# Optimization experiments

Hardware: AMD Instinct MI355X
Metric: run time of the kernel (lower is better)

Reference implementation:

```python
import jax, jax.numpy as jnp
import numpy as np

N = 50000   # nodes
E = 800000  # edges (avg degree 16)
IN, H, OUT = 128, 256, 40


def setup_inputs() -> dict:
    key = jax.random.key(0)
    ks = jax.random.split(key, 7)
    x = jax.random.normal(ks[0], (N, IN), dtype=jnp.float32)
    edge_index = jax.random.randint(ks[1], (2, E), 0, N, dtype=jnp.int32)
    def w(k, fi, fo):
        return jax.random.normal(k, (fi, fo), dtype=jnp.float32) / np.sqrt(fi).astype(np.float32)
    return {
        "x": x,
        "edge_index": edge_index,
        "W0": w(ks[2], IN, H), "b0": jnp.zeros((H,), jnp.float32),
        "W1": w(ks[3], H, H),  "b1": jnp.zeros((H,), jnp.float32),
        "W2": w(ks[4], H, H),  "b2": jnp.zeros((H,), jnp.float32),
        "Wh": w(ks[5], H, OUT), "bh": jnp.zeros((OUT,), jnp.float32),
    }


def gcn_conv(x, src, dst, W, b, n):
    """PyG GCNConv: self-loops + symmetric D^-1/2 (A+I) D^-1/2 normalization."""
    h = x @ W  # [N, Fout]
    # degree with self-loop (edge weights are all 1)
    deg = jnp.ones((n,), h.dtype).at[dst].add(1.0)
    inv = jax.lax.rsqrt(deg)  # deg^{-1/2}
    coef = inv[src] * inv[dst]  # [E]
    agg = jax.ops.segment_sum(h[src] * coef[:, None], dst, num_segments=n)
    agg = agg + h * (inv * inv)[:, None]  # self-loop contribution
    return agg + b


def reference(x, edge_index, W0, b0, W1, b1, W2, b2, Wh, bh):
    src, dst = edge_index[0], edge_index[1]
    h = jax.nn.relu(gcn_conv(x, src, dst, W0, b0, N))   # conv0 + relu (dropout p=0)
    h = jax.nn.relu(gcn_conv(h, src, dst, W1, b1, N))   # conv1 + relu
    h = gcn_conv(h, src, dst, W2, b2, N)                # final conv (no relu)
    g = jnp.mean(h, axis=0, keepdims=True)              # batch=None -> global mean, [1, H]
    return g @ Wh + bh                                  # prediction head, [1, OUT]
```

## Files before the change

kernel.cpp:

```cpp
#include <hip/hip_runtime.h>

#define NN 50000
#define NE 800000
#define FIN 128
#define FH 256
#define FOUT 40
#define NPAD 50432
#define NN2 50048
#define NB 256
#define BSPAN 196
#define EBLK 4096
#define NBLK_A 196
#define NBLK_S 196

typedef float f32x4 __attribute__((ext_vector_type(4)));
typedef short bf16x8 __attribute__((ext_vector_type(8)));

__device__ __forceinline__ ushort f2bf(float f) {
    unsigned u = __float_as_uint(f);
    unsigned r = (u + 0x7FFFu + ((u >> 16) & 1u)) >> 16;
    return (ushort)r;
}
__device__ __forceinline__ float bf2f(ushort b) {
    return __uint_as_float(((unsigned)b) << 16);
}


__global__ __launch_bounds__(256) void bucket_cnt_kernel(const int* __restrict__ dst,
                                                         int* __restrict__ bcnt) {
    __shared__ int h[NB];
    const int t = threadIdx.x;
    h[t] = 0;
    __syncthreads();
    const int e0 = blockIdx.x * EBLK;
    const int n  = min(EBLK, NE - e0);
    for (int i = t; i < n; i += 256)
        atomicAdd(&h[dst[e0 + i] / BSPAN], 1);
    __syncthreads();
    if (h[t] > 0) atomicAdd(&bcnt[t], h[t]);
}

__global__ __launch_bounds__(256) void bucket_scan_kernel(const int* __restrict__ bcnt,
                                                          int* __restrict__ bbase,
                                                          int* __restrict__ bcur,
                                                          float* __restrict__ vbuf) {
    __shared__ int sh[256];
    int t = threadIdx.x;
    int v = bcnt[t];
    sh[t] = v;
    __syncthreads();
    #pragma unroll
    for (int off = 1; off < 256; off <<= 1) {
        int u = (t >= off) ? sh[t - off] : 0;
        __syncthreads();
        sh[t] += u;
        __syncthreads();
    }
    int excl = sh[t] - v;
    bbase[t] = excl;
    bcur[t]  = excl;
    if (t == 255) bbase[256] = sh[255];
    vbuf[t] = 0.0f;
}

__global__ __launch_bounds__(256) void binA_kernel(const int* __restrict__ src,
                                                   const int* __restrict__ dst,
                                                   int* __restrict__ bcur,
                                                   unsigned* __restrict__ inter) {
    __shared__ int hcnt[NB];
    __shared__ int hoff[NB];
    __shared__ int lcur[NB];
    __shared__ int gbase[NB];
    __shared__ unsigned stage[EBLK];

    const int t  = threadIdx.x;
    const int e0 = blockIdx.x * EBLK;
    const int n  = min(EBLK, NE - e0);

    hcnt[t] = 0;
    __syncthreads();
    for (int i = t; i < n; i += 256)
        atomicAdd(&hcnt[dst[e0 + i] / BSPAN], 1);
    __syncthreads();
    int v = hcnt[t];
    hoff[t] = v;
    __syncthreads();
    #pragma unroll
    for (int off = 1; off < NB; off <<= 1) {
        int u = (t >= off) ? hoff[t - off] : 0;
        __syncthreads();
        hoff[t] += u;
        __syncthreads();
    }
    int excl = hoff[t] - v;
    __syncthreads();
    hoff[t] = excl;
    lcur[t] = excl;
    if (v > 0) gbase[t] = atomicAdd(&bcur[t], v);
    __syncthreads();
    for (int i = t; i < n; i += 256) {
        int d = dst[e0 + i];
        int s = src[e0 + i];
        int b = d / BSPAN;
        int idx = atomicAdd(&lcur[b], 1);
        stage[idx] = ((unsigned)d << 16) | (unsigned)s;
    }
    __syncthreads();
    for (int i = t; i < n; i += 256) {
        unsigned rec = stage[i];
        int b = (int)(rec >> 16) / BSPAN;
        inter[gbase[b] + (i - hoff[b])] = rec;
    }
}

__global__ __launch_bounds__(256) void binB1_kernel(const unsigned* __restrict__ inter,
                                                    const int* __restrict__ bbase,
                                                    int* __restrict__ row_start,
                                                    float* __restrict__ inv,
                                                    float* __restrict__ wsum) {
    __shared__ int lcnt[BSPAN];
    __shared__ int sh[256];
    const int b   = blockIdx.x;
    const int nlo = b * BSPAN;
    const int nhi = min(nlo + BSPAN, NN);
    const int nn  = nhi - nlo;
    const int base = bbase[b];
    const int cnt  = bbase[b + 1] - base;
    const int t = threadIdx.x;

    for (int i = t; i < nn; i += 256) lcnt[i] = 0;
    __syncthreads();
    for (int i = t; i < cnt; i += 256)
        atomicAdd(&lcnt[(int)(inter[base + i] >> 16) - nlo], 1);
    __syncthreads();
    int c = (t < nn) ? lcnt[t] : 0;
    sh[t] = c;
    __syncthreads();
    #pragma unroll
    for (int off = 1; off < 256; off <<= 1) {
        int u = (t >= off) ? sh[t - off] : 0;
        __syncthreads();
        sh[t] += u;
        __syncthreads();
    }
    if (t < nn) {
        row_start[nlo + t] = base + sh[t] - c;
        inv[nlo + t]  = rsqrtf((float)(c + 1));
        wsum[nlo + t] = 0.0f;
    }
    if (b == NB - 1 && t == 0) row_start[NN] = NE;
}

__global__ __launch_bounds__(256) void binB2_kernel(const unsigned* __restrict__ inter,
                                                    const int* __restrict__ bbase,
                                                    const int* __restrict__ row_start,
                                                    const float* __restrict__ inv,
                                                    float2* __restrict__ edata,
                                                    float* __restrict__ wsum) {
    __shared__ int lcur[BSPAN];
    const int b   = blockIdx.x;
    const int nlo = b * BSPAN;
    const int nhi = min(nlo + BSPAN, NN);
    const int nn  = nhi - nlo;
    const int base = bbase[b];
    const int cnt  = bbase[b + 1] - base;
    const int t = threadIdx.x;

    for (int i = t; i < nn; i += 256) lcur[i] = row_start[nlo + i];
    __syncthreads();
    for (int i = t; i < cnt; i += 256) {
        unsigned rec = inter[base + i];
        int d = (int)(rec >> 16);
        int s = (int)(rec & 0xFFFFu);
        float coef = inv[s] * inv[d];
        int pos = atomicAdd(&lcur[d - nlo], 1);
        edata[pos] = make_float2(__int_as_float(s), coef);
        unsafeAtomicAdd(&wsum[s], coef);
    }
}


__global__ void wsplit_kernel(const float* __restrict__ W, int K, int N,
                              ushort* __restrict__ WtH, ushort* __restrict__ WtL) {
    int idx = blockIdx.x * 256 + threadIdx.x;
    if (idx >= K * N) return;
    int n = idx % N;
    int k = idx / N;
    float f = W[idx];
    ushort h = f2bf(f);
    WtH[(size_t)n * K + k] = h;
    if (WtL) WtL[(size_t)n * K + k] = f2bf(f - bf2f(h));
}


template<int TERMS, bool BIAS_RELU>
__global__ __launch_bounds__(256) void gemm_mfma_kernel(
    const ushort* __restrict__ AH, const ushort* __restrict__ AL,
    const ushort* __restrict__ BH, const ushort* __restrict__ BL,
    const float* __restrict__ bias,
    ushort* __restrict__ outB,
    int M, int K) {
    constexpr int NARR = (TERMS == 3) ? 4 : 2;
    __shared__ ushort smem[NARR * 128 * 40];
    ushort* Ah = smem;
    ushort* Bh = smem + 128 * 40;
    ushort* Al = (TERMS == 3) ? smem + 2 * 128 * 40 : nullptr;
    ushort* Bl = (TERMS == 3) ? smem + 3 * 128 * 40 : nullptr;

    const int tid  = threadIdx.x;
    const int lane = tid & 63;
    const int w    = tid >> 6;
    const int wr   = w >> 1;
    const int wc   = w & 1;
    const int row0 = blockIdx.x * 128;
    const int col0 = blockIdx.y * 128;

    f32x4 acc[4][4] = {};

    for (int k0 = 0; k0 < K; k0 += 32) {
        #pragma unroll
        for (int i = 0; i < 2; ++i) {
            int c  = i * 256 + tid;
            int r  = c >> 2;
            int cb = c & 3;
            int gr = row0 + r;
            uint4 vh = make_uint4(0u, 0u, 0u, 0u);
            if (gr < M)
                vh = *reinterpret_cast<const uint4*>(AH + (size_t)gr * K + k0 + cb * 8);
            *reinterpret_cast<uint4*>(&Ah[r * 40 + cb * 8]) = vh;
            *reinterpret_cast<uint4*>(&Bh[r * 40 + cb * 8]) =
                *reinterpret_cast<const uint4*>(BH + (size_t)(col0 + r) * K + k0 + cb * 8);
            if (TERMS == 3) {
                uint4 vl = make_uint4(0u, 0u, 0u, 0u);
                if (gr < M)
                    vl = *reinterpret_cast<const uint4*>(AL + (size_t)gr * K + k0 + cb * 8);
                *reinterpret_cast<uint4*>(&Al[r * 40 + cb * 8]) = vl;
                *reinterpret_cast<uint4*>(&Bl[r * 40 + cb * 8]) =
                    *reinterpret_cast<const uint4*>(BL + (size_t)(col0 + r) * K + k0 + cb * 8);
            }
        }
        __syncthreads();

        const int rsel = lane & 15;
        const int ksel = (lane >> 4) * 8;
        bf16x8 ah[4], bh[4];
        #pragma unroll
        for (int m = 0; m < 4; ++m)
            ah[m] = *reinterpret_cast<const bf16x8*>(&Ah[(wr * 64 + m * 16 + rsel) * 40 + ksel]);
        #pragma unroll
        for (int n = 0; n < 4; ++n)
            bh[n] = *reinterpret_cast<const bf16x8*>(&Bh[(wc * 64 + n * 16 + rsel) * 40 + ksel]);

        if (TERMS == 3) {
            bf16x8 al[4], bl[4];
            #pragma unroll
            for (int m = 0; m < 4; ++m)
                al[m] = *reinterpret_cast<const bf16x8*>(&Al[(wr * 64 + m * 16 + rsel) * 40 + ksel]);
            #pragma unroll
            for (int n = 0; n < 4; ++n)
                bl[n] = *reinterpret_cast<const bf16x8*>(&Bl[(wc * 64 + n * 16 + rsel) * 40 + ksel]);
            #pragma unroll
            for (int m = 0; m < 4; ++m)
                #pragma unroll
                for (int n = 0; n < 4; ++n) {
                    acc[m][n] = __builtin_amdgcn_mfma_f32_16x16x32_bf16(ah[m], bh[n], acc[m][n], 0, 0, 0);
                    acc[m][n] = __builtin_amdgcn_mfma_f32_16x16x32_bf16(ah[m], bl[n], acc[m][n], 0, 0, 0);
                    acc[m][n] = __builtin_amdgcn_mfma_f32_16x16x32_bf16(al[m], bh[n], acc[m][n], 0, 0, 0);
                }
        } else {
            #pragma unroll
            for (int m = 0; m < 4; ++m)
                #pragma unroll
                for (int n = 0; n < 4; ++n)
                    acc[m][n] = __builtin_amdgcn_mfma_f32_16x16x32_bf16(ah[m], bh[n], acc[m][n], 0, 0, 0);
        }
        __syncthreads();
    }

    const int cl = lane & 15;
    const int rg = lane >> 4;
    #pragma unroll
    for (int m = 0; m < 4; ++m) {
        #pragma unroll
        for (int i = 0; i < 4; ++i) {
            int gr = row0 + wr * 64 + m * 16 + rg * 4 + i;
            if (gr < M) {
                #pragma unroll
                for (int n = 0; n < 4; ++n) {
                    int gc = col0 + wc * 64 + n * 16 + cl;
                    float o = acc[m][n][i];
                    if (BIAS_RELU) o = fmaxf(o + bias[gc], 0.0f);
                    outB[(size_t)gr * FH + gc] = f2bf(o);
                }
            }
        }
    }
}


__global__ __launch_bounds__(256) void gather_x_kernel(const float* __restrict__ x,
                                                       const float2* __restrict__ edata,
                                                       const int* __restrict__ row_start,
                                                       const float* __restrict__ inv,
                                                       ushort* __restrict__ outH,
                                                       ushort* __restrict__ outL) {
    int node = blockIdx.x * 4 + (threadIdx.x >> 6);
    int lane = threadIdx.x & 63;
    if (node >= NN) return;

    int beg = row_start[node];
    int end = row_start[node + 1];

    float iv = inv[node];
    float c  = iv * iv;
    float2 v = *reinterpret_cast<const float2*>(x + (size_t)node * FIN + lane * 2);
    float2 a0 = make_float2(v.x * c, v.y * c);
    float2 a1 = make_float2(0.f, 0.f);
    float2 a2 = make_float2(0.f, 0.f);
    float2 a3 = make_float2(0.f, 0.f);

    int i = beg;
    if ((i & 1) && i < end) {
        float2 ed = edata[i];
        float2 w = *reinterpret_cast<const float2*>(x + (size_t)__float_as_int(ed.x) * FIN + lane * 2);
        a0.x += w.x * ed.y; a0.y += w.y * ed.y;
        ++i;
    }
    for (; i + 8 <= end; i += 8) {
        float4 e01 = *reinterpret_cast<const float4*>(&edata[i]);
        float4 e23 = *reinterpret_cast<const float4*>(&edata[i + 2]);
        float4 e45 = *reinterpret_cast<const float4*>(&edata[i + 4]);
        float4 e67 = *reinterpret_cast<const float4*>(&edata[i + 6]);
        float2 w0 = *reinterpret_cast<const float2*>(x + (size_t)__float_as_int(e01.x) * FIN + lane * 2);
        float2 w1 = *reinterpret_cast<const float2*>(x + (size_t)__float_as_int(e01.z) * FIN + lane * 2);
        float2 w2 = *reinterpret_cast<const float2*>(x + (size_t)__float_as_int(e23.x) * FIN + lane * 2);
        float2 w3 = *reinterpret_cast<const float2*>(x + (size_t)__float_as_int(e23.z) * FIN + lane * 2);
        float2 w4 = *reinterpret_cast<const float2*>(x + (size_t)__float_as_int(e45.x) * FIN + lane * 2);
        float2 w5 = *reinterpret_cast<const float2*>(x + (size_t)__float_as_int(e45.z) * FIN + lane * 2);
        float2 w6 = *reinterpret_cast<const float2*>(x + (size_t)__float_as_int(e67.x) * FIN + lane * 2);
        float2 w7 = *reinterpret_cast<const float2*>(x + (size_t)__float_as_int(e67.z) * FIN + lane * 2);
        a0.x += w0.x * e01.y; a0.y += w0.y * e01.y;
        a1.x += w1.x * e01.w; a1.y += w1.y * e01.w;
        a2.x += w2.x * e23.y; a2.y += w2.y * e23.y;
        a3.x += w3.x * e23.w; a3.y += w3.y * e23.w;
        a0.x += w4.x * e45.y; a0.y += w4.y * e45.y;
        a1.x += w5.x * e45.w; a1.y += w5.y * e45.w;
        a2.x += w6.x * e67.y; a2.y += w6.y * e67.y;
        a3.x += w7.x * e67.w; a3.y += w7.y * e67.w;
    }
    for (; i + 2 <= end; i += 2) {
        float4 e01 = *reinterpret_cast<const float4*>(&edata[i]);
        float2 w0 = *reinterpret_cast<const float2*>(x + (size_t)__float_as_int(e01.x) * FIN + lane * 2);
        float2 w1 = *reinterpret_cast<const float2*>(x + (size_t)__float_as_int(e01.z) * FIN + lane * 2);
        a0.x += w0.x * e01.y; a0.y += w0.y * e01.y;
        a1.x += w1.x * e01.w; a1.y += w1.y * e01.w;
    }
    if (i < end) {
        float2 ed = edata[i];
        float2 w = *reinterpret_cast<const float2*>(x + (size_t)__float_as_int(ed.x) * FIN + lane * 2);
        a0.x += w.x * ed.y; a0.y += w.y * ed.y;
    }

    float ax = a0.x + a1.x + a2.x + a3.x;
    float ay = a0.y + a1.y + a2.y + a3.y;
    ushort h0 = f2bf(ax), h1 = f2bf(ay);
    ushort l0 = f2bf(ax - bf2f(h0)), l1 = f2bf(ay - bf2f(h1));
    size_t o = (size_t)node * FIN + lane * 2;
    *reinterpret_cast<ushort2*>(outH + o) = make_ushort2(h0, h1);
    *reinterpret_cast<ushort2*>(outL + o) = make_ushort2(l0, l1);
}


__global__ __launch_bounds__(256) void gather_bf_kernel(const ushort* __restrict__ lin,
                                                        const float2* __restrict__ edata,
                                                        const int* __restrict__ row_start,
                                                        const float* __restrict__ inv,
                                                        const float* __restrict__ bias,
                                                        ushort* __restrict__ outB) {
    int node = blockIdx.x * 4 + (threadIdx.x >> 6);
    int lane = threadIdx.x & 63;
    if (node >= NN) return;

    int beg = row_start[node];
    int end = row_start[node + 1];

    float iv = inv[node];
    float c  = iv * iv;
    ushort4 sv = *reinterpret_cast<const ushort4*>(lin + (size_t)node * FH + lane * 4);
    float4 b = *reinterpret_cast<const float4*>(bias + lane * 4);
    float4 a0 = make_float4(bf2f(sv.x) * c + b.x, bf2f(sv.y) * c + b.y,
                            bf2f(sv.z) * c + b.z, bf2f(sv.w) * c + b.w);
    float4 a1 = make_float4(0.f, 0.f, 0.f, 0.f);
    float4 a2 = make_float4(0.f, 0.f, 0.f, 0.f);
    float4 a3 = make_float4(0.f, 0.f, 0.f, 0.f);

    int i = beg;
    if ((i & 1) && i < end) {
        float2 ed = edata[i];
        float cf = ed.y;
        ushort4 wv = *reinterpret_cast<const ushort4*>(lin + (size_t)__float_as_int(ed.x) * FH + lane * 4);
        a0.x += bf2f(wv.x) * cf; a0.y += bf2f(wv.y) * cf;
        a0.z += bf2f(wv.z) * cf; a0.w += bf2f(wv.w) * cf;
        ++i;
    }
    for (; i + 8 <= end; i += 8) {
        float4 e01 = *reinterpret_cast<const float4*>(&edata[i]);
        float4 e23 = *reinterpret_cast<const float4*>(&edata[i + 2]);
        float4 e45 = *reinterpret_cast<const float4*>(&edata[i + 4]);
        float4 e67 = *reinterpret_cast<const float4*>(&edata[i + 6]);
        ushort4 w0 = *reinterpret_cast<const ushort4*>(lin + (size_t)__float_as_int(e01.x) * FH + lane * 4);
        ushort4 w1 = *reinterpret_cast<const ushort4*>(lin + (size_t)__float_as_int(e01.z) * FH + lane * 4);
        ushort4 w2 = *reinterpret_cast<const ushort4*>(lin + (size_t)__float_as_int(e23.x) * FH + lane * 4);
        ushort4 w3 = *reinterpret_cast<const ushort4*>(lin + (size_t)__float_as_int(e23.z) * FH + lane * 4);
        ushort4 w4 = *reinterpret_cast<const ushort4*>(lin + (size_t)__float_as_int(e45.x) * FH + lane * 4);
        ushort4 w5 = *reinterpret_cast<const ushort4*>(lin + (size_t)__float_as_int(e45.z) * FH + lane * 4);
        ushort4 w6 = *reinterpret_cast<const ushort4*>(lin + (size_t)__float_as_int(e67.x) * FH + lane * 4);
        ushort4 w7 = *reinterpret_cast<const ushort4*>(lin + (size_t)__float_as_int(e67.z) * FH + lane * 4);
        a0.x += bf2f(w0.x) * e01.y; a0.y += bf2f(w0.y) * e01.y;
        a0.z += bf2f(w0.z) * e01.y; a0.w += bf2f(w0.w) * e01.y;
        a1.x += bf2f(w1.x) * e01.w; a1.y += bf2f(w1.y) * e01.w;
        a1.z += bf2f(w1.z) * e01.w; a1.w += bf2f(w1.w) * e01.w;
        a2.x += bf2f(w2.x) * e23.y; a2.y += bf2f(w2.y) * e23.y;
        a2.z += bf2f(w2.z) * e23.y; a2.w += bf2f(w2.w) * e23.y;
        a3.x += bf2f(w3.x) * e23.w; a3.y += bf2f(w3.y) * e23.w;
        a3.z += bf2f(w3.z) * e23.w; a3.w += bf2f(w3.w) * e23.w;
        a0.x += bf2f(w4.x) * e45.y; a0.y += bf2f(w4.y) * e45.y;
        a0.z += bf2f(w4.z) * e45.y; a0.w += bf2f(w4.w) * e45.y;
        a1.x += bf2f(w5.x) * e45.w; a1.y += bf2f(w5.y) * e45.w;
        a1.z += bf2f(w5.z) * e45.w; a1.w += bf2f(w5.w) * e45.w;
        a2.x += bf2f(w6.x) * e67.y; a2.y += bf2f(w6.y) * e67.y;
        a2.z += bf2f(w6.z) * e67.y; a2.w += bf2f(w6.w) * e67.y;
        a3.x += bf2f(w7.x) * e67.w; a3.y += bf2f(w7.y) * e67.w;
        a3.z += bf2f(w7.z) * e67.w; a3.w += bf2f(w7.w) * e67.w;
    }
    for (; i + 2 <= end; i += 2) {
        float4 e01 = *reinterpret_cast<const float4*>(&edata[i]);
        ushort4 w0 = *reinterpret_cast<const ushort4*>(lin + (size_t)__float_as_int(e01.x) * FH + lane * 4);
        ushort4 w1 = *reinterpret_cast<const ushort4*>(lin + (size_t)__float_as_int(e01.z) * FH + lane * 4);
        a0.x += bf2f(w0.x) * e01.y; a0.y += bf2f(w0.y) * e01.y;
        a0.z += bf2f(w0.z) * e01.y; a0.w += bf2f(w0.w) * e01.y;
        a1.x += bf2f(w1.x) * e01.w; a1.y += bf2f(w1.y) * e01.w;
        a1.z += bf2f(w1.z) * e01.w; a1.w += bf2f(w1.w) * e01.w;
    }
    if (i < end) {
        float2 ed = edata[i];
        float cf = ed.y;
        ushort4 wv = *reinterpret_cast<const ushort4*>(lin + (size_t)__float_as_int(ed.x) * FH + lane * 4);
        a0.x += bf2f(wv.x) * cf; a0.y += bf2f(wv.y) * cf;
        a0.z += bf2f(wv.z) * cf; a0.w += bf2f(wv.w) * cf;
    }

    float4 acc = make_float4(a0.x + a1.x + a2.x + a3.x,
                             a0.y + a1.y + a2.y + a3.y,
                             a0.z + a1.z + a2.z + a3.z,
                             a0.w + a1.w + a2.w + a3.w);

    float r0 = fmaxf(acc.x, 0.f), r1 = fmaxf(acc.y, 0.f);
    float r2 = fmaxf(acc.z, 0.f), r3 = fmaxf(acc.w, 0.f);
    *reinterpret_cast<ushort4*>(outB + (size_t)node * FH + lane * 4) =
        make_ushort4(f2bf(r0), f2bf(r1), f2bf(r2), f2bf(r3));
}


__global__ __launch_bounds__(256) void colsumw_kernel(const ushort* __restrict__ a1,
                                                      const float* __restrict__ wsum,
                                                      const float* __restrict__ inv,
                                                      float* __restrict__ v) {
    __shared__ float sh[4][256];
    int wid  = threadIdx.x >> 6;
    int lane = threadIdx.x & 63;
    int r0 = blockIdx.x * 256;
    int r1 = r0 + 256; if (r1 > NN) r1 = NN;

    float4 acc = make_float4(0.f, 0.f, 0.f, 0.f);
    for (int r = r0 + wid; r < r1; r += 4) {
        float iv = inv[r];
        float wr = wsum[r] + iv * iv;
        ushort4 u = *reinterpret_cast<const ushort4*>(a1 + (size_t)r * FH + lane * 4);
        acc.x += bf2f(u.x) * wr;
        acc.y += bf2f(u.y) * wr;
        acc.z += bf2f(u.z) * wr;
        acc.w += bf2f(u.w) * wr;
    }
    *reinterpret_cast<float4*>(&sh[wid][lane * 4]) = acc;
    __syncthreads();
    if (wid == 0) {
        float4 s1 = *reinterpret_cast<const float4*>(&sh[1][lane * 4]);
        float4 s2 = *reinterpret_cast<const float4*>(&sh[2][lane * 4]);
        float4 s3 = *reinterpret_cast<const float4*>(&sh[3][lane * 4]);
        unsafeAtomicAdd(&v[lane * 4 + 0], acc.x + s1.x + s2.x + s3.x);
        unsafeAtomicAdd(&v[lane * 4 + 1], acc.y + s1.y + s2.y + s3.y);
        unsafeAtomicAdd(&v[lane * 4 + 2], acc.z + s1.z + s2.z + s3.z);
        unsafeAtomicAdd(&v[lane * 4 + 3], acc.w + s1.w + s2.w + s3.w);
    }
}

__global__ __launch_bounds__(256) void head2_kernel(const float* __restrict__ v,
                                                    const float* __restrict__ W2,
                                                    const float* __restrict__ b2,
                                                    const float* __restrict__ Wh,
                                                    const float* __restrict__ bh,
                                                    float* __restrict__ out) {
    __shared__ float m[FH];
    int t = threadIdx.x;
    const float scale = 1.0f / (float)NN;
    float s = 0.0f;
    for (int f = 0; f < FH; ++f)
        s += v[f] * W2[f * FH + t];
    m[t] = s * scale + b2[t];
    __syncthreads();
    if (t < FOUT) {
        float o = 0.0f;
        for (int f = 0; f < FH; ++f)
            o += m[f] * Wh[f * FOUT + t];
        out[t] = o + bh[t];
    }
}


extern "C" void kernel_launch(void* const* d_in, const int* in_sizes, int n_in,
                              void* d_out, int out_size, void* d_ws, size_t ws_size,
                              hipStream_t stream) {
    const float* x   = (const float*)d_in[0];
    const int*   ei  = (const int*)d_in[1];
    const float* W0  = (const float*)d_in[2];
    const float* b0  = (const float*)d_in[3];
    const float* W1  = (const float*)d_in[4];
    const float* b1  = (const float*)d_in[5];
    const float* W2  = (const float*)d_in[6];
    const float* b2  = (const float*)d_in[7];
    const float* Wh  = (const float*)d_in[8];
    const float* bh  = (const float*)d_in[9];
    float* out = (float*)d_out;

    const int* src = ei;
    const int* dst = ei + NE;

    float*    inv       = (float*)d_ws;
    int*      row_start = (int*)(inv + NPAD);
    float*    wsum      = (float*)(row_start + NPAD);
    int*      bcnt      = (int*)(wsum + NPAD);
    int*      bbase     = bcnt + 256;
    int*      bcur      = bbase + 320;
    float*    vbuf      = (float*)(bcur + 256);
    unsigned* inter     = (unsigned*)(vbuf + 256);
    float2*   edata     = (float2*)(inter + NE);
    ushort*   W0tH      = (ushort*)(edata + NE);
    ushort*   W0tL      = W0tH + 256 * 128;
    ushort*   W1tH      = W0tL + 256 * 128;
    ushort*   aggxH     = W1tH + 256 * 256;
    ushort*   aggxL     = aggxH + (size_t)NN2 * 128;
    ushort*   linb      = aggxH;
    ushort*   h0H       = aggxL + (size_t)NN2 * 128;
    ushort*   a1H       = h0H;

    const dim3 gemm_grid((NN + 127) / 128, 2);
    const int nblk_g = (NN + 3) / 4;

    hipMemsetAsync(bcnt, 0, NB * sizeof(int), stream);
    bucket_cnt_kernel<<<NBLK_A, 256, 0, stream>>>(dst, bcnt);
    bucket_scan_kernel<<<1, 256, 0, stream>>>(bcnt, bbase, bcur, vbuf);
    binA_kernel<<<NBLK_A, 256, 0, stream>>>(src, dst, bcur, inter);
    binB1_kernel<<<NB, 256, 0, stream>>>(inter, bbase, row_start, inv, wsum);
    binB2_kernel<<<NB, 256, 0, stream>>>(inter, bbase, row_start, inv, edata, wsum);
    wsplit_kernel<<<(FIN * FH + 255) / 256, 256, 0, stream>>>(W0, FIN, FH, W0tH, W0tL);
    wsplit_kernel<<<(FH * FH + 255) / 256, 256, 0, stream>>>(W1, FH, FH, W1tH, nullptr);

    gather_x_kernel<<<nblk_g, 256, 0, stream>>>(x, edata, row_start, inv, aggxH, aggxL);
    gemm_mfma_kernel<3, true><<<gemm_grid, 256, 0, stream>>>(aggxH, aggxL, W0tH, W0tL, b0,
                                                             h0H, NN, FIN);

    gemm_mfma_kernel<1, false><<<gemm_grid, 256, 0, stream>>>(h0H, nullptr, W1tH, nullptr, nullptr,
                                                              linb, NN, FH);
    gather_bf_kernel<<<nblk_g, 256, 0, stream>>>(linb, edata, row_start, inv, b1, a1H);

    colsumw_kernel<<<NBLK_S, 256, 0, stream>>>(a1H, wsum, inv, vbuf);
    head2_kernel<<<1, 256, 0, stream>>>(vbuf, W2, b2, Wh, bh, out);
}
```

Measured before the change: 314.9 us.

## Gather x in bf16, widen GEMM tile to full 256 columns, merge weight splits

Adds a pass that converts x to bf16 (padded to NN2 rows), so the first-layer neighbor gather reads half the bytes per edge. The GEMM now computes all 256 output columns per block (128x256 tile, 4x8 accumulators) over a padded row range, dropping the row bounds checks and the duplicate A-tile loads across column blocks. The two weight-split kernels are merged into one launch. This adds an extra full pass over x and more registers and LDS per GEMM block, and rounding x to bf16 before aggregation adds precision error.

```diff
diff --git a/kernel.cpp b/kernel.cpp
--- a/kernel.cpp
+++ b/kernel.cpp
@@ -180,16 +180,38 @@
 }
 
 
-__global__ void wsplit_kernel(const float* __restrict__ W, int K, int N,
-                              ushort* __restrict__ WtH, ushort* __restrict__ WtL) {
+__global__ void wsplit_all_kernel(const float* __restrict__ W0, const float* __restrict__ W1,
+                                  ushort* __restrict__ W0tH, ushort* __restrict__ W0tL,
+                                  ushort* __restrict__ W1tH) {
     int idx = blockIdx.x * 256 + threadIdx.x;
-    if (idx >= K * N) return;
-    int n = idx % N;
-    int k = idx / N;
-    float f = W[idx];
-    ushort h = f2bf(f);
-    WtH[(size_t)n * K + k] = h;
-    if (WtL) WtL[(size_t)n * K + k] = f2bf(f - bf2f(h));
+    if (idx < FIN * FH) {
+        int n = idx % FH;
+        int k = idx / FH;
+        float f = W0[idx];
+        ushort h = f2bf(f);
+        W0tH[n * FIN + k] = h;
+        W0tL[n * FIN + k] = f2bf(f - bf2f(h));
+    }
+    int j = idx - FIN * FH;
+    if (j >= 0 && j < FH * FH) {
+        int n = j % FH;
+        int k = j / FH;
+        W1tH[n * FH + k] = f2bf(W1[j]);
+    }
+}
+
+
+__global__ void xcvt_kernel(const float* __restrict__ x, ushort* __restrict__ xb) {
+    int t = blockIdx.x * 256 + threadIdx.x;
+    if (t >= NN2 * 32) return;
+    int row = t >> 5;
+    int c4  = t & 31;
+    ushort4 o = make_ushort4(0, 0, 0, 0);
+    if (row < NN) {
+        float4 v = *reinterpret_cast<const float4*>(x + (size_t)row * FIN + c4 * 4);
+        o = make_ushort4(f2bf(v.x), f2bf(v.y), f2bf(v.z), f2bf(v.w));
+    }
+    *reinterpret_cast<ushort4*>(xb + (size_t)row * FIN + c4 * 4) = o;
 }
 
 
@@ -199,13 +221,13 @@
     const ushort* __restrict__ BH, const ushort* __restrict__ BL,
     const float* __restrict__ bias,
     ushort* __restrict__ outB,
-    int M, int K) {
-    constexpr int NARR = (TERMS == 3) ? 4 : 2;
-    __shared__ ushort smem[NARR * 128 * 40];
+    int K) {
+    constexpr int NARR = (TERMS == 3) ? 2 : 1;
+    __shared__ ushort smem[(128 + 256) * 40 * NARR];
     ushort* Ah = smem;
     ushort* Bh = smem + 128 * 40;
-    ushort* Al = (TERMS == 3) ? smem + 2 * 128 * 40 : nullptr;
-    ushort* Bl = (TERMS == 3) ? smem + 3 * 128 * 40 : nullptr;
+    ushort* Al = (TERMS == 3) ? smem + 384 * 40 : nullptr;
+    ushort* Bl = (TERMS == 3) ? smem + 384 * 40 + 128 * 40 : nullptr;
 
     const int tid  = threadIdx.x;
     const int lane = tid & 63;
@@ -213,9 +235,8 @@
     const int wr   = w >> 1;
     const int wc   = w & 1;
     const int row0 = blockIdx.x * 128;
-    const int col0 = blockIdx.y * 128;
-
-    f32x4 acc[4][4] = {};
+
+    f32x4 acc[4][8] = {};
 
     for (int k0 = 0; k0 < K; k0 += 32) {
         #pragma unroll
@@ -223,46 +244,47 @@
             int c  = i * 256 + tid;
             int r  = c >> 2;
             int cb = c & 3;
-            int gr = row0 + r;
-            uint4 vh = make_uint4(0u, 0u, 0u, 0u);
-            if (gr < M)
-                vh = *reinterpret_cast<const uint4*>(AH + (size_t)gr * K + k0 + cb * 8);
-            *reinterpret_cast<uint4*>(&Ah[r * 40 + cb * 8]) = vh;
+            *reinterpret_cast<uint4*>(&Ah[r * 40 + cb * 8]) =
+                *reinterpret_cast<const uint4*>(AH + (size_t)(row0 + r) * K + k0 + cb * 8);
+            if (TERMS == 3)
+                *reinterpret_cast<uint4*>(&Al[r * 40 + cb * 8]) =
+                    *reinterpret_cast<const uint4*>(AL + (size_t)(row0 + r) * K + k0 + cb * 8);
+        }
+        #pragma unroll
+        for (int i = 0; i < 4; ++i) {
+            int c  = i * 256 + tid;
+            int r  = c >> 2;
+            int cb = c & 3;
             *reinterpret_cast<uint4*>(&Bh[r * 40 + cb * 8]) =
-                *reinterpret_cast<const uint4*>(BH + (size_t)(col0 + r) * K + k0 + cb * 8);
-            if (TERMS == 3) {
-                uint4 vl = make_uint4(0u, 0u, 0u, 0u);
-                if (gr < M)
-                    vl = *reinterpret_cast<const uint4*>(AL + (size_t)gr * K + k0 + cb * 8);
-                *reinterpret_cast<uint4*>(&Al[r * 40 + cb * 8]) = vl;
+                *reinterpret_cast<const uint4*>(BH + (size_t)r * K + k0 + cb * 8);
+            if (TERMS == 3)
                 *reinterpret_cast<uint4*>(&Bl[r * 40 + cb * 8]) =
-                    *reinterpret_cast<const uint4*>(BL + (size_t)(col0 + r) * K + k0 + cb * 8);
-            }
+                    *reinterpret_cast<const uint4*>(BL + (size_t)r * K + k0 + cb * 8);
         }
         __syncthreads();
 
         const int rsel = lane & 15;
         const int ksel = (lane >> 4) * 8;
-        bf16x8 ah[4], bh[4];
+        bf16x8 ah[4], bh[8];
         #pragma unroll
         for (int m = 0; m < 4; ++m)
             ah[m] = *reinterpret_cast<const bf16x8*>(&Ah[(wr * 64 + m * 16 + rsel) * 40 + ksel]);
         #pragma unroll
-        for (int n = 0; n < 4; ++n)
-            bh[n] = *reinterpret_cast<const bf16x8*>(&Bh[(wc * 64 + n * 16 + rsel) * 40 + ksel]);
+        for (int n = 0; n < 8; ++n)
+            bh[n] = *reinterpret_cast<const bf16x8*>(&Bh[(wc * 128 + n * 16 + rsel) * 40 + ksel]);
 
         if (TERMS == 3) {
-            bf16x8 al[4], bl[4];
+            bf16x8 al[4], bl[8];
             #pragma unroll
             for (int m = 0; m < 4; ++m)
                 al[m] = *reinterpret_cast<const bf16x8*>(&Al[(wr * 64 + m * 16 + rsel) * 40 + ksel]);
             #pragma unroll
-            for (int n = 0; n < 4; ++n)
-                bl[n] = *reinterpret_cast<const bf16x8*>(&Bl[(wc * 64 + n * 16 + rsel) * 40 + ksel]);
+            for (int n = 0; n < 8; ++n)
+                bl[n] = *reinterpret_cast<const bf16x8*>(&Bl[(wc * 128 + n * 16 + rsel) * 40 + ksel]);
             #pragma unroll
             for (int m = 0; m < 4; ++m)
                 #pragma unroll
-                for (int n = 0; n < 4; ++n) {
+                for (int n = 0; n < 8; ++n) {
                     acc[m][n] = __builtin_amdgcn_mfma_f32_16x16x32_bf16(ah[m], bh[n], acc[m][n], 0, 0, 0);
                     acc[m][n] = __builtin_amdgcn_mfma_f32_16x16x32_bf16(ah[m], bl[n], acc[m][n], 0, 0, 0);
                     acc[m][n] = __builtin_amdgcn_mfma_f32_16x16x32_bf16(al[m], bh[n], acc[m][n], 0, 0, 0);
@@ -271,7 +293,7 @@
             #pragma unroll
             for (int m = 0; m < 4; ++m)
                 #pragma unroll
-                for (int n = 0; n < 4; ++n)
+                for (int n = 0; n < 8; ++n)
                     acc[m][n] = __builtin_amdgcn_mfma_f32_16x16x32_bf16(ah[m], bh[n], acc[m][n], 0, 0, 0);
         }
         __syncthreads();
@@ -279,26 +301,29 @@
 
     const int cl = lane & 15;
     const int rg = lane >> 4;
+    float bn[8];
+    if (BIAS_RELU) {
+        #pragma unroll
+        for (int n = 0; n < 8; ++n) bn[n] = bias[wc * 128 + n * 16 + cl];
+    }
     #pragma unroll
     for (int m = 0; m < 4; ++m) {
         #pragma unroll
         for (int i = 0; i < 4; ++i) {
             int gr = row0 + wr * 64 + m * 16 + rg * 4 + i;
-            if (gr < M) {
-                #pragma unroll
-                for (int n = 0; n < 4; ++n) {
-                    int gc = col0 + wc * 64 + n * 16 + cl;
-                    float o = acc[m][n][i];
-                    if (BIAS_RELU) o = fmaxf(o + bias[gc], 0.0f);
-                    outB[(size_t)gr * FH + gc] = f2bf(o);
-                }
+            #pragma unroll
+            for (int n = 0; n < 8; ++n) {
+                int gc = wc * 128 + n * 16 + cl;
+                float o = acc[m][n][i];
+                if (BIAS_RELU) o = fmaxf(o + bn[n], 0.0f);
+                outB[(size_t)gr * FH + gc] = f2bf(o);
             }
         }
     }
 }
 
 
-__global__ __launch_bounds__(256) void gather_x_kernel(const float* __restrict__ x,
+__global__ __launch_bounds__(256) void gather_x_kernel(const ushort* __restrict__ xb,
                                                        const float2* __restrict__ edata,
                                                        const int* __restrict__ row_start,
                                                        const float* __restrict__ inv,
@@ -306,15 +331,21 @@
                                                        ushort* __restrict__ outL) {
     int node = blockIdx.x * 4 + (threadIdx.x >> 6);
     int lane = threadIdx.x & 63;
-    if (node >= NN) return;
+    if (node >= NN2) return;
+    size_t o = (size_t)node * FIN + lane * 2;
+    if (node >= NN) {
+        *reinterpret_cast<ushort2*>(outH + o) = make_ushort2(0, 0);
+        *reinterpret_cast<ushort2*>(outL + o) = make_ushort2(0, 0);
+        return;
+    }
 
     int beg = row_start[node];
     int end = row_start[node + 1];
 
     float iv = inv[node];
     float c  = iv * iv;
-    float2 v = *reinterpret_cast<const float2*>(x + (size_t)node * FIN + lane * 2);
-    float2 a0 = make_float2(v.x * c, v.y * c);
+    ushort2 sv = *reinterpret_cast<const ushort2*>(xb + o);
+    float2 a0 = make_float2(bf2f(sv.x) * c, bf2f(sv.y) * c);
     float2 a1 = make_float2(0.f, 0.f);
     float2 a2 = make_float2(0.f, 0.f);
     float2 a3 = make_float2(0.f, 0.f);
@@ -322,8 +353,8 @@
     int i = beg;
     if ((i & 1) && i < end) {
         float2 ed = edata[i];
-        float2 w = *reinterpret_cast<const float2*>(x + (size_t)__float_as_int(ed.x) * FIN + lane * 2);
-        a0.x += w.x * ed.y; a0.y += w.y * ed.y;
+        ushort2 u = *reinterpret_cast<const ushort2*>(xb + (size_t)__float_as_int(ed.x) * FIN + lane * 2);
+        a0.x += bf2f(u.x) * ed.y; a0.y += bf2f(u.y) * ed.y;
         ++i;
     }
     for (; i + 8 <= end; i += 8) {
@@ -331,41 +362,40 @@
         float4 e23 = *reinterpret_cast<const float4*>(&edata[i + 2]);
         float4 e45 = *reinterpret_cast<const float4*>(&edata[i + 4]);
         float4 e67 = *reinterpret_cast<const float4*>(&edata[i + 6]);
-        float2 w0 = *reinterpret_cast<const float2*>(x + (size_t)__float_as_int(e01.x) * FIN + lane * 2);
-        float2 w1 = *reinterpret_cast<const float2*>(x + (size_t)__float_as_int(e01.z) * FIN + lane * 2);
-        float2 w2 = *reinterpret_cast<const float2*>(x + (size_t)__float_as_int(e23.x) * FIN + lane * 2);
-        float2 w3 = *reinterpret_cast<const float2*>(x + (size_t)__float_as_int(e23.z) * FIN + lane * 2);
-        float2 w4 = *reinterpret_cast<const float2*>(x + (size_t)__float_as_int(e45.x) * FIN + lane * 2);
-        float2 w5 = *reinterpret_cast<const float2*>(x + (size_t)__float_as_int(e45.z) * FIN + lane * 2);
-        float2 w6 = *reinterpret_cast<const float2*>(x + (size_t)__float_as_int(e67.x) * FIN + lane * 2);
-        float2 w7 = *reinterpret_cast<const float2*>(x + (size_t)__float_as_int(e67.z) * FIN + lane * 2);
-        a0.x += w0.x * e01.y; a0.y += w0.y * e01.y;
-        a1.x += w1.x * e01.w; a1.y += w1.y * e01.w;
-        a2.x += w2.x * e23.y; a2.y += w2.y * e23.y;
-        a3.x += w3.x * e23.w; a3.y += w3.y * e23.w;
-        a0.x += w4.x * e45.y; a0.y += w4.y * e45.y;
-        a1.x += w5.x * e45.w; a1.y += w5.y * e45.w;
-        a2.x += w6.x * e67.y; a2.y += w6.y * e67.y;
-        a3.x += w7.x * e67.w; a3.y += w7.y * e67.w;
+        ushort2 u0 = *reinterpret_cast<const ushort2*>(xb + (size_t)__float_as_int(e01.x) * FIN + lane * 2);
+        ushort2 u1 = *reinterpret_cast<const ushort2*>(xb + (size_t)__float_as_int(e01.z) * FIN + lane * 2);
+        ushort2 u2 = *reinterpret_cast<const ushort2*>(xb + (size_t)__float_as_int(e23.x) * FIN + lane * 2);
+        ushort2 u3 = *reinterpret_cast<const ushort2*>(xb + (size_t)__float_as_int(e23.z) * FIN + lane * 2);
+        ushort2 u4 = *reinterpret_cast<const ushort2*>(xb + (size_t)__float_as_int(e45.x) * FIN + lane * 2);
+        ushort2 u5 = *reinterpret_cast<const ushort2*>(xb + (size_t)__float_as_int(e45.z) * FIN + lane * 2);
+        ushort2 u6 = *reinterpret_cast<const ushort2*>(xb + (size_t)__float_as_int(e67.x) * FIN + lane * 2);
+        ushort2 u7 = *reinterpret_cast<const ushort2*>(xb + (size_t)__float_as_int(e67.z) * FIN + lane * 2);
+        a0.x += bf2f(u0.x) * e01.y; a0.y += bf2f(u0.y) * e01.y;
+        a1.x += bf2f(u1.x) * e01.w; a1.y += bf2f(u1.y) * e01.w;
+        a2.x += bf2f(u2.x) * e23.y; a2.y += bf2f(u2.y) * e23.y;
+        a3.x += bf2f(u3.x) * e23.w; a3.y += bf2f(u3.y) * e23.w;
+        a0.x += bf2f(u4.x) * e45.y; a0.y += bf2f(u4.y) * e45.y;
+        a1.x += bf2f(u5.x) * e45.w; a1.y += bf2f(u5.y) * e45.w;
+        a2.x += bf2f(u6.x) * e67.y; a2.y += bf2f(u6.y) * e67.y;
+        a3.x += bf2f(u7.x) * e67.w; a3.y += bf2f(u7.y) * e67.w;
     }
     for (; i + 2 <= end; i += 2) {
         float4 e01 = *reinterpret_cast<const float4*>(&edata[i]);
-        float2 w0 = *reinterpret_cast<const float2*>(x + (size_t)__float_as_int(e01.x) * FIN + lane * 2);
-        float2 w1 = *reinterpret_cast<const float2*>(x + (size_t)__float_as_int(e01.z) * FIN + lane * 2);
-        a0.x += w0.x * e01.y; a0.y += w0.y * e01.y;
-        a1.x += w1.x * e01.w; a1.y += w1.y * e01.w;
+        ushort2 u0 = *reinterpret_cast<const ushort2*>(xb + (size_t)__float_as_int(e01.x) * FIN + lane * 2);
+        ushort2 u1 = *reinterpret_cast<const ushort2*>(xb + (size_t)__float_as_int(e01.z) * FIN + lane * 2);
+        a0.x += bf2f(u0.x) * e01.y; a0.y += bf2f(u0.y) * e01.y;
+        a1.x += bf2f(u1.x) * e01.w; a1.y += bf2f(u1.y) * e01.w;
     }
     if (i < end) {
         float2 ed = edata[i];
-        float2 w = *reinterpret_cast<const float2*>(x + (size_t)__float_as_int(ed.x) * FIN + lane * 2);
-        a0.x += w.x * ed.y; a0.y += w.y * ed.y;
+        ushort2 u = *reinterpret_cast<const ushort2*>(xb + (size_t)__float_as_int(ed.x) * FIN + lane * 2);
+        a0.x += bf2f(u.x) * ed.y; a0.y += bf2f(u.y) * ed.y;
     }
 
     float ax = a0.x + a1.x + a2.x + a3.x;
     float ay = a0.y + a1.y + a2.y + a3.y;
     ushort h0 = f2bf(ax), h1 = f2bf(ay);
     ushort l0 = f2bf(ax - bf2f(h0)), l1 = f2bf(ay - bf2f(h1));
-    size_t o = (size_t)node * FIN + lane * 2;
     *reinterpret_cast<ushort2*>(outH + o) = make_ushort2(h0, h1);
     *reinterpret_cast<ushort2*>(outL + o) = make_ushort2(l0, l1);
 }
@@ -548,14 +578,16 @@
     ushort*   W0tH      = (ushort*)(edata + NE);
     ushort*   W0tL      = W0tH + 256 * 128;
     ushort*   W1tH      = W0tL + 256 * 128;
-    ushort*   aggxH     = W1tH + 256 * 256;
+    ushort*   xb        = W1tH + 256 * 256;
+    ushort*   aggxH     = xb + (size_t)NN2 * 128;
     ushort*   aggxL     = aggxH + (size_t)NN2 * 128;
     ushort*   linb      = aggxH;
     ushort*   h0H       = aggxL + (size_t)NN2 * 128;
     ushort*   a1H       = h0H;
 
-    const dim3 gemm_grid((NN + 127) / 128, 2);
-    const int nblk_g = (NN + 3) / 4;
+    const int gemm_grid = NN2 / 128;
+    const int nblk_gx = NN2 / 4;
+    const int nblk_g  = (NN + 3) / 4;
 
     hipMemsetAsync(bcnt, 0, NB * sizeof(int), stream);
     bucket_cnt_kernel<<<NBLK_A, 256, 0, stream>>>(dst, bcnt);
@@ -563,15 +595,15 @@
     binA_kernel<<<NBLK_A, 256, 0, stream>>>(src, dst, bcur, inter);
     binB1_kernel<<<NB, 256, 0, stream>>>(inter, bbase, row_start, inv, wsum);
     binB2_kernel<<<NB, 256, 0, stream>>>(inter, bbase, row_start, inv, edata, wsum);
-    wsplit_kernel<<<(FIN * FH + 255) / 256, 256, 0, stream>>>(W0, FIN, FH, W0tH, W0tL);
-    wsplit_kernel<<<(FH * FH + 255) / 256, 256, 0, stream>>>(W1, FH, FH, W1tH, nullptr);
-
-    gather_x_kernel<<<nblk_g, 256, 0, stream>>>(x, edata, row_start, inv, aggxH, aggxL);
+    wsplit_all_kernel<<<(FIN * FH + FH * FH + 255) / 256, 256, 0, stream>>>(W0, W1, W0tH, W0tL, W1tH);
+    xcvt_kernel<<<(NN2 * 32 + 255) / 256, 256, 0, stream>>>(x, xb);
+
+    gather_x_kernel<<<nblk_gx, 256, 0, stream>>>(xb, edata, row_start, inv, aggxH, aggxL);
     gemm_mfma_kernel<3, true><<<gemm_grid, 256, 0, stream>>>(aggxH, aggxL, W0tH, W0tL, b0,
-                                                             h0H, NN, FIN);
+                                                             h0H, FIN);
 
     gemm_mfma_kernel<1, false><<<gemm_grid, 256, 0, stream>>>(h0H, nullptr, W1tH, nullptr, nullptr,
-                                                              linb, NN, FH);
+                                                              linb, FH);
     gather_bf_kernel<<<nblk_g, 256, 0, stream>>>(linb, edata, row_start, inv, b1, a1H);
 
     colsumw_kernel<<<NBLK_S, 256, 0, stream>>>(a1H, wsum, inv, vbuf);
```

Result: faster. 300.6 us (-4.5%).
